# Kernel tuning notes

Measured on AMD Instinct MI355X. Metric: run time of the kernel, lower is better.

Reference implementation:

```python
import jax, jax.numpy as jnp
import numpy as np

EPS = 1e-5

def conv3(x, w, b):
    # 3x3 conv, stride 1, pad 1, NCHW/OIHW
    y = jax.lax.conv_general_dilated(x, w, (1, 1), ((1, 1), (1, 1)),
                                     dimension_numbers=('NCHW', 'OIHW', 'NCHW'))
    return y + b[None, :, None, None]

def positional_norm(x):
    # per-pixel channel-wise norm; torch .var() is unbiased (ddof=1)
    mean = jnp.mean(x, axis=1, keepdims=True)
    var = jnp.var(x, axis=1, keepdims=True, ddof=1)
    return (x - mean) / jnp.sqrt(var + EPS)

def bilinear_gather(x, py, px):
    # x: [B,C,H,W]; py/px: [B,K,H,W] absolute sample coords -> [B,C,K,H,W]
    B, C, H, W = x.shape
    K = py.shape[1]
    xf = x.reshape(B, C, H * W)
    y0 = jnp.floor(py).astype(jnp.int32)
    x0 = jnp.floor(px).astype(jnp.int32)
    wy = py - y0.astype(x.dtype)
    wx = px - x0.astype(x.dtype)

    def corner(yi, xi):
        valid = ((yi >= 0) & (yi < H) & (xi >= 0) & (xi < W)).astype(x.dtype)
        idx = (jnp.clip(yi, 0, H - 1) * W + jnp.clip(xi, 0, W - 1)).reshape(B, 1, K * H * W)
        v = jnp.take_along_axis(xf, idx, axis=2).reshape(B, C, K, H, W)
        return v * valid[:, None]

    out = ((1 - wy) * (1 - wx))[:, None] * corner(y0, x0)
    out = out + ((1 - wy) * wx)[:, None] * corner(y0, x0 + 1)
    out = out + (wy * (1 - wx))[:, None] * corner(y0 + 1, x0)
    out = out + (wy * wx)[:, None] * corner(y0 + 1, x0 + 1)
    return out

def dcn_v2(feat, cond, w_off, b_off, w_dcn, b_dcn):
    # DCNv2Pack: conv_offset(cond) -> (o1, o2, mask); modulated deformable 3x3 conv on feat
    B, C, H, W = feat.shape
    om = conv3(cond, w_off, b_off)                      # [B, 27, H, W]
    off = om[:, :18].reshape(B, 9, 2, H, W)             # (dy, dx) per kernel tap
    mask = jax.nn.sigmoid(om[:, 18:])                   # [B, 9, H, W]
    dy, dx = off[:, :, 0], off[:, :, 1]
    ki = jnp.repeat(jnp.arange(-1.0, 2.0, dtype=feat.dtype), 3)   # tap row offsets
    kj = jnp.tile(jnp.arange(-1.0, 2.0, dtype=feat.dtype), 3)     # tap col offsets
    hh = jnp.arange(H, dtype=feat.dtype)
    ww = jnp.arange(W, dtype=feat.dtype)
    py = dy + hh[None, None, :, None] + ki[None, :, None, None]
    px = dx + ww[None, None, None, :] + kj[None, :, None, None]
    sampled = bilinear_gather(feat, py, px)             # [B,C,9,H,W]
    wk = w_dcn.reshape(w_dcn.shape[0], C, 9)
    out = jnp.einsum('bkhw,bckhw,ock->bohw', mask, sampled, wk)
    return out + b_dcn[None, :, None, None]

def spade_forward(x, ref, w1, b1, w2, b2, w_off, b_off, w_dcn, b_dcn, w_g, b_g, w_be, b_be):
    normalized = positional_norm(x)
    h = jax.nn.relu(conv3(jnp.concatenate((normalized, ref), axis=1), w1, b1))
    cond = jax.nn.relu(conv3(h, w2, b2))
    ref_refine = dcn_v2(ref, cond, w_off, b_off, w_dcn, b_dcn)
    gamma = conv3(ref_refine, w_g, b_g)
    beta = conv3(ref_refine, w_be, b_be)
    return normalized * (1 + gamma) + beta

def setup_inputs() -> dict:
    key = jax.random.key(0)
    ks = jax.random.split(key, 16)
    B, NC, SC, H, W = 2, 64, 64, 96, 96
    mid = (NC + SC) // 8  # 16
    s = 0.05
    inp = {
        'x': jax.random.normal(ks[0], (B, NC, H, W), jnp.float32),
        'ref': jax.random.normal(ks[1], (B, SC, H, W), jnp.float32),
        'w1': jax.random.normal(ks[2], (mid, NC + SC, 3, 3), jnp.float32) * s,
        'b1': jax.random.normal(ks[3], (mid,), jnp.float32) * s,
        'w2': jax.random.normal(ks[4], (SC, mid, 3, 3), jnp.float32) * s,
        'b2': jax.random.normal(ks[5], (SC,), jnp.float32) * s,
        'w_off': jax.random.normal(ks[6], (27, SC, 3, 3), jnp.float32) * 0.01,
        'b_off': jax.random.normal(ks[7], (27,), jnp.float32) * 0.01,
        'w_dcn': jax.random.normal(ks[8], (SC, SC, 3, 3), jnp.float32) * s,
        'b_dcn': jax.random.normal(ks[9], (SC,), jnp.float32) * s,
        'w_g': jax.random.normal(ks[10], (NC, SC, 3, 3), jnp.float32) * s,
        'b_g': jax.random.normal(ks[11], (NC,), jnp.float32) * s,
        'w_be': jax.random.normal(ks[12], (NC, SC, 3, 3), jnp.float32) * s,
        'b_be': jax.random.normal(ks[13], (NC,), jnp.float32) * s,
    }
    return inp

def reference(x, ref, w1, b1, w2, b2, w_off, b_off, w_dcn, b_dcn, w_g, b_g, w_be, b_be):
    return spade_forward(x, ref, w1, b1, w2, b2, w_off, b_off, w_dcn, b_dcn, w_g, b_g, w_be, b_be)
```

## Files before the change

kernel.cpp:

```cpp
#include <hip/hip_runtime.h>
#include <math.h>

namespace {

typedef __attribute__((ext_vector_type(8))) short          bf16x8;
typedef __attribute__((ext_vector_type(8))) unsigned short u16x8;
typedef __attribute__((ext_vector_type(4))) float          f32x4;

constexpr int B_  = 2;
constexpr int H_  = 96;
constexpr int W_  = 96;
constexpr int HW_ = H_ * W_;
constexpr int NC_ = 64;
constexpr int SC_ = 64;

__device__ inline unsigned short f2bf(float f) {
    union { float f; unsigned u; } v; v.f = f;
    unsigned r = v.u + 0x7FFFu + ((v.u >> 16) & 1u);
    return (unsigned short)(r >> 16);
}
__device__ inline float bf2f(unsigned short s) {
    union { unsigned u; float f; } v; v.u = ((unsigned)s) << 16; return v.f;
}
__device__ inline bf16x8 ld_frag(const unsigned short* p) {
    return *reinterpret_cast<const bf16x8*>(p);
}

__global__ __launch_bounds__(256)
void prologue(const float* __restrict__ x, const float* __restrict__ ref,
              const float* __restrict__ w1, const float* __restrict__ w2,
              const float* __restrict__ woff, const float* __restrict__ wg,
              const float* __restrict__ wbe, const float* __restrict__ wdcn,
              float* __restrict__ nrm, unsigned short* __restrict__ cc,
              unsigned short* __restrict__ wt1, unsigned short* __restrict__ wt2,
              unsigned short* __restrict__ wtoff, unsigned short* __restrict__ wtg,
              unsigned short* __restrict__ wtbe, unsigned short* __restrict__ wbd) {
    __shared__ float red1[4][64];
    __shared__ float red2[4][64];
    __shared__ float rtile[64][65];

    int blk = blockIdx.x;
    int t   = threadIdx.x;

    if (blk < 288) {
        int b  = blk / 144;
        int p0 = (blk % 144) * 64;
        int px = t & 63;
        int cg = t >> 6;
        int p  = p0 + px;

        float v[16];
        float s1 = 0.f, s2 = 0.f;
        const float* xb = x + ((size_t)b * NC_ + cg * 16) * HW_ + p;
        #pragma unroll
        for (int j = 0; j < 16; ++j) {
            v[j] = xb[j * HW_];
            s1 += v[j];
            s2 = fmaf(v[j], v[j], s2);
        }
        red1[cg][px] = s1;
        red2[cg][px] = s2;

        const float* rb = ref + (size_t)b * SC_ * HW_ + p0 + px;
        #pragma unroll
        for (int it = 0; it < 16; ++it) {
            int ch = it * 4 + cg;
            rtile[ch][px] = rb[(size_t)ch * HW_];
        }
        __syncthreads();

        s1 = red1[0][px] + red1[1][px] + red1[2][px] + red1[3][px];
        s2 = red2[0][px] + red2[1][px] + red2[2][px] + red2[3][px];
        float mean = s1 * (1.f / 64.f);
        float var  = (s2 - 64.f * mean * mean) * (1.f / 63.f);
        float inv  = 1.f / sqrtf(var + 1e-5f);
        float* nb = nrm + ((size_t)b * NC_ + cg * 16) * HW_ + p;
        u16x8 pk[2];
        #pragma unroll
        for (int j = 0; j < 16; ++j) {
            float nv = (v[j] - mean) * inv;
            nb[j * HW_] = nv;
            pk[j >> 3][j & 7] = f2bf(nv);
        }
        size_t bp = (size_t)b * HW_ + p;
        *reinterpret_cast<u16x8*>(&cc[bp * 128 + cg * 16 + 0]) = pk[0];
        *reinterpret_cast<u16x8*>(&cc[bp * 128 + cg * 16 + 8]) = pk[1];

        {
            int wpx = t >> 2, q = t & 3;
            size_t bp2 = (size_t)b * HW_ + p0 + wpx;
            u16x8 o0, o1;
            #pragma unroll
            for (int j = 0; j < 8; ++j) {
                o0[j] = f2bf(rtile[q * 16 + j][wpx]);
                o1[j] = f2bf(rtile[q * 16 + 8 + j][wpx]);
            }
            *reinterpret_cast<u16x8*>(&cc[bp2 * 128 + 64 + q * 16 + 0]) = o0;
            *reinterpret_cast<u16x8*>(&cc[bp2 * 128 + 64 + q * 16 + 8]) = o1;
        }
    } else {
        int idx = (blk - 288) * 256 + t;
        if (idx < 9 * 16 * 128) {
            int tap = idx / (16 * 128), oc = (idx / 128) % 16, ic = idx % 128;
            wt1[idx] = f2bf(w1[(oc * 128 + ic) * 9 + tap]);
        }
        if (idx < 9 * 64 * 32) {
            int tap = idx / (64 * 32), oc = (idx / 32) % 64, ic = idx % 32;
            wt2[idx] = (ic < 16) ? f2bf(w2[(oc * 16 + ic) * 9 + tap]) : (unsigned short)0;
        }
        if (idx < 9 * 32 * 64) {
            int tap = idx / (32 * 64), oc = (idx / 64) % 32, ic = idx % 64;
            wtoff[idx] = (oc < 27) ? f2bf(woff[(oc * 64 + ic) * 9 + tap]) : (unsigned short)0;
        }
        if (idx < 9 * 64 * 64) {
            int tap = idx / (64 * 64), oc = (idx / 64) % 64, ic = idx % 64;
            wtg[idx]  = f2bf(wg [(oc * 64 + ic) * 9 + tap]);
            wtbe[idx] = f2bf(wbe[(oc * 64 + ic) * 9 + tap]);
        }
        if (idx < 64 * 576) {
            int oc = idx / 576, r = idx - oc * 576;
            int tap = r >> 6, ic = r & 63;
            wbd[idx] = f2bf(wdcn[oc * 576 + ic * 9 + tap]);
        }
    }
}

template <int ICS, int ICP, int COLP, int COUT_PAD, int COUT_REAL,
          bool DUAL, bool RELU, int OMODE>
__global__ __launch_bounds__(256)
void conv_bf(const unsigned short* __restrict__ in,
             const unsigned short* __restrict__ Wt,
             const unsigned short* __restrict__ Wt2,
             const float* __restrict__ bias, const float* __restrict__ bias2,
             const float* __restrict__ nrm, float* __restrict__ outF,
             unsigned short* __restrict__ outB) {
    constexpr int NOCT = COUT_PAD / 16;
    constexpr int WPO  = 4 / NOCT;
    constexpr int MTP  = NOCT;
    constexpr int NACC = DUAL ? 2 : 1;
    constexpr int NKS  = ICP / 32;
    constexpr int NCH8 = ICP / 8;

    __shared__ unsigned short patch[6 * 18 * COLP];

    int t   = threadIdx.x;
    int blk = blockIdx.x;
    int bx  = blk % 6;
    int by  = (blk / 6) % 24;
    int b   = blk / 144;
    int x0  = bx * 16, y0 = by * 4;

    for (int e = t; e < 6 * 18 * NCH8; e += 256) {
        int kc  = e % NCH8;
        int col = (e / NCH8) % 18;
        int row = e / (NCH8 * 18);
        int yy = y0 + row - 1, xx = x0 + col - 1;
        bf16x8 v = (bf16x8){0, 0, 0, 0, 0, 0, 0, 0};
        if (kc * 8 < ICS && (unsigned)yy < (unsigned)H_ && (unsigned)xx < (unsigned)W_) {
            v = ld_frag(&in[((size_t)b * HW_ + yy * W_ + xx) * ICS + kc * 8]);
        }
        *reinterpret_cast<bf16x8*>(&patch[(row * 18 + col) * COLP + kc * 8]) = v;
    }
    __syncthreads();

    int wave = t >> 6, lane = t & 63;
    int fr = lane & 15, fq = lane >> 4;
    int oct  = wave / WPO;
    int widx = wave - oct * WPO;
    int mt0  = widx * MTP;

    f32x4 acc[MTP][NACC];
    #pragma unroll
    for (int i = 0; i < MTP; ++i)
        #pragma unroll
        for (int a = 0; a < NACC; ++a)
            acc[i][a] = (f32x4){0.f, 0.f, 0.f, 0.f};

    constexpr int dyv[9] = {0,0,0,1,1,1,2,2,2};
    constexpr int dxv[9] = {0,1,2,0,1,2,0,1,2};

    #pragma unroll
    for (int tap = 0; tap < 9; ++tap) {
        int dy = dyv[tap], dx = dxv[tap];
        #pragma unroll
        for (int ks = 0; ks < NKS; ++ks) {
            const size_t wo = ((size_t)tap * COUT_PAD + oct * 16 + fr) * ICP + ks * 32 + fq * 8;
            bf16x8 wfA = ld_frag(&Wt[wo]);
            bf16x8 wfB;
            if (DUAL) wfB = ld_frag(&Wt2[wo]);
            #pragma unroll
            for (int i = 0; i < MTP; ++i) {
                bf16x8 pf = ld_frag(&patch[((mt0 + i + dy) * 18 + (fr + dx)) * COLP
                                           + ks * 32 + fq * 8]);
                acc[i][0] = __builtin_amdgcn_mfma_f32_16x16x32_bf16(wfA, pf, acc[i][0], 0, 0, 0);
                if (DUAL)
                    acc[i][1] = __builtin_amdgcn_mfma_f32_16x16x32_bf16(wfB, pf, acc[i][1], 0, 0, 0);
            }
        }
    }

    #pragma unroll
    for (int i = 0; i < MTP; ++i) {
        int py = mt0 + i;
        if (OMODE == 1) {
            size_t p = (size_t)b * HW_ + (size_t)(y0 + py) * W_ + x0 + fr;
            ushort4 sv;
            #pragma unroll
            for (int j = 0; j < 4; ++j) {
                float v = acc[i][0][j] + bias[oct * 16 + fq * 4 + j];
                if (RELU) v = fmaxf(v, 0.f);
                ((unsigned short*)&sv)[j] = f2bf(v);
            }
            *reinterpret_cast<ushort4*>(&outB[p * COUT_REAL + oct * 16 + fq * 4]) = sv;
        } else if (OMODE == 2) {
            size_t p = (size_t)b * HW_ + (size_t)(y0 + py) * W_ + x0 + fr;
            float4 o4;
            #pragma unroll
            for (int j = 0; j < 4; ++j) {
                int oc = oct * 16 + fq * 4 + j;
                float v = acc[i][0][j] + (oc < COUT_REAL ? bias[oc] : 0.f);
                ((float*)&o4)[j] = v;
            }
            *reinterpret_cast<float4*>(&outF[p * 32 + oct * 16 + fq * 4]) = o4;
        } else {
            #pragma unroll
            for (int j = 0; j < 4; ++j) {
                int oc = oct * 16 + fq * 4 + j;
                if (oc >= COUT_REAL) continue;
                size_t off = ((size_t)b * COUT_REAL + oc) * HW_
                           + (size_t)(y0 + py) * W_ + x0 + fr;
                float v = acc[i][0][j] + bias[oc];
                if (DUAL) {
                    float be = acc[i][1][j] + bias2[oc];
                    float nv = nrm[off];
                    outF[off] = fmaf(nv, 1.f + v, be);
                } else {
                    outF[off] = RELU ? fmaxf(v, 0.f) : v;
                }
            }
        }
    }
}

constexpr int SROW = 584;

__global__ __launch_bounds__(256)
void dcn_kernel(const unsigned short* __restrict__ cc, const float* __restrict__ omP,
                const unsigned short* __restrict__ wbd, const float* __restrict__ b_dcn,
                unsigned short* __restrict__ rrT) {
    __shared__ unsigned short sS[16 * SROW];
    __shared__ float4 cwL[144];
    __shared__ int4   ciL[144];

    int t  = threadIdx.x;
    int b  = blockIdx.x / 576;
    int p0 = (blockIdx.x % 576) * 16;

    const unsigned short* ccb = cc + (size_t)b * HW_ * 128;

    if (t < 144) {
        int pp = t / 9, k = t - pp * 9;
        int p  = p0 + pp;
        int y  = p / W_, x = p - y * W_;
        const float* omp = &omP[(size_t)(b * HW_ + p) * 32];
        float dy = omp[2 * k];
        float dx = omp[2 * k + 1];
        float mk = omp[18 + k];
        mk = 1.f / (1.f + expf(-mk));

        float py = dy + (float)y + (float)(k / 3 - 1);
        float px = dx + (float)x + (float)(k % 3 - 1);
        float fy = floorf(py), fx = floorf(px);
        int   y0 = (int)fy,   x0 = (int)fx;
        float wy = py - fy,   wx = px - fx;

        float cw[4];
        int   ci[4];
        #pragma unroll
        for (int i = 0; i < 4; ++i) {
            int yy = y0 + (i >> 1);
            int xx = x0 + (i & 1);
            bool valid = (yy >= 0) && (yy < H_) && (xx >= 0) && (xx < W_);
            int yc = yy < 0 ? 0 : (yy > H_ - 1 ? H_ - 1 : yy);
            int xc = xx < 0 ? 0 : (xx > W_ - 1 ? W_ - 1 : xx);
            ci[i] = yc * W_ + xc;
            float wyi = (i >> 1) ? wy : (1.f - wy);
            float wxi = (i & 1)  ? wx : (1.f - wx);
            cw[i] = valid ? mk * wyi * wxi : 0.f;
        }
        cwL[t] = make_float4(cw[0], cw[1], cw[2], cw[3]);
        ciL[t] = make_int4(ci[0], ci[1], ci[2], ci[3]);
    }
    __syncthreads();

    {
        int pp = t >> 4, cg = t & 15;
        #pragma unroll
        for (int k = 0; k < 9; ++k) {
            float4 cw = cwL[pp * 9 + k];
            int4   ci = ciL[pp * 9 + k];
            ushort4 r0 = *reinterpret_cast<const ushort4*>(&ccb[(size_t)ci.x * 128 + 64 + cg * 4]);
            ushort4 r1 = *reinterpret_cast<const ushort4*>(&ccb[(size_t)ci.y * 128 + 64 + cg * 4]);
            ushort4 r2 = *reinterpret_cast<const ushort4*>(&ccb[(size_t)ci.z * 128 + 64 + cg * 4]);
            ushort4 r3 = *reinterpret_cast<const ushort4*>(&ccb[(size_t)ci.w * 128 + 64 + cg * 4]);
            float vx = cw.x * bf2f(r0.x) + cw.y * bf2f(r1.x) + cw.z * bf2f(r2.x) + cw.w * bf2f(r3.x);
            float vy = cw.x * bf2f(r0.y) + cw.y * bf2f(r1.y) + cw.z * bf2f(r2.y) + cw.w * bf2f(r3.y);
            float vz = cw.x * bf2f(r0.z) + cw.y * bf2f(r1.z) + cw.z * bf2f(r2.z) + cw.w * bf2f(r3.z);
            float vw = cw.x * bf2f(r0.w) + cw.y * bf2f(r1.w) + cw.z * bf2f(r2.w) + cw.w * bf2f(r3.w);
            ushort4 sv;
            sv.x = f2bf(vx); sv.y = f2bf(vy); sv.z = f2bf(vz); sv.w = f2bf(vw);
            *reinterpret_cast<ushort4*>(&sS[pp * SROW + k * 64 + cg * 4]) = sv;
        }
    }
    __syncthreads();

    int wave = t >> 6, lane = t & 63;
    int fr = lane & 15, fq = lane >> 4;

    f32x4 acc = (f32x4){0.f, 0.f, 0.f, 0.f};
    for (int ks = 0; ks < 18; ++ks) {
        bf16x8 wf = ld_frag(&wbd[(size_t)(wave * 16 + fr) * 576 + ks * 32 + fq * 8]);
        bf16x8 pf = ld_frag(&sS[(size_t)fr * SROW + ks * 32 + fq * 8]);
        acc = __builtin_amdgcn_mfma_f32_16x16x32_bf16(wf, pf, acc, 0, 0, 0);
    }

    {
        size_t p = (size_t)b * HW_ + p0 + fr;
        ushort4 sv;
        #pragma unroll
        for (int j = 0; j < 4; ++j)
            ((unsigned short*)&sv)[j] = f2bf(acc[j] + b_dcn[wave * 16 + fq * 4 + j]);
        *reinterpret_cast<ushort4*>(&rrT[p * 64 + wave * 16 + fq * 4]) = sv;
    }
}

}

extern "C" void kernel_launch(void* const* d_in, const int* in_sizes, int n_in,
                              void* d_out, int out_size, void* d_ws, size_t ws_size,
                              hipStream_t stream) {
    (void)in_sizes; (void)n_in; (void)out_size; (void)ws_size;

    const float* x     = (const float*)d_in[0];
    const float* ref   = (const float*)d_in[1];
    const float* w1    = (const float*)d_in[2];
    const float* b1    = (const float*)d_in[3];
    const float* w2    = (const float*)d_in[4];
    const float* b2    = (const float*)d_in[5];
    const float* w_off = (const float*)d_in[6];
    const float* b_off = (const float*)d_in[7];
    const float* w_dcn = (const float*)d_in[8];
    const float* b_dcn = (const float*)d_in[9];
    const float* w_g   = (const float*)d_in[10];
    const float* b_g   = (const float*)d_in[11];
    const float* w_be  = (const float*)d_in[12];
    const float* b_be  = (const float*)d_in[13];

    float* out = (float*)d_out;
    float* ws  = (float*)d_ws;

    float* nrm = ws;
    float* omP = nrm + 1179648;
    unsigned short* cc    = (unsigned short*)(omP + 589824);
    unsigned short* hmidT = cc    + 2359296;
    unsigned short* condT = hmidT + 294912;
    unsigned short* rrT   = condT + 1179648;
    unsigned short* wt1   = rrT   + 1179648;
    unsigned short* wt2   = wt1   + 18432;
    unsigned short* wtoff = wt2   + 18432;
    unsigned short* wtg   = wtoff + 18432;
    unsigned short* wtbe  = wtg   + 36864;
    unsigned short* wbd   = wtbe  + 36864;

    prologue<<<432, 256, 0, stream>>>(x, ref, w1, w2, w_off, w_g, w_be, w_dcn,
                                      nrm, cc, wt1, wt2, wtoff, wtg, wtbe, wbd);

    constexpr int GRID = 288;

    conv_bf<128, 128, 136, 16, 16, false, true, 1>
        <<<GRID, 256, 0, stream>>>(cc, wt1, nullptr, b1, nullptr, nullptr, nullptr, hmidT);

    conv_bf<16, 32, 40, 64, 64, false, true, 1>
        <<<GRID, 256, 0, stream>>>(hmidT, wt2, nullptr, b2, nullptr, nullptr, nullptr, condT);

    conv_bf<64, 64, 72, 32, 27, false, false, 2>
        <<<GRID, 256, 0, stream>>>(condT, wtoff, nullptr, b_off, nullptr, nullptr, omP, nullptr);

    dcn_kernel<<<B_ * 576, 256, 0, stream>>>(cc, omP, wbd, b_dcn, rrT);

    conv_bf<64, 64, 72, 64, 64, true, false, 0>
        <<<GRID, 256, 0, stream>>>(rrT, wtg, wtbe, b_g, b_be, nrm, out, nullptr);
}
```

Measured before the change: 73.76 us.

## Double DCN pixel tile to 32, widen gathers to 16B, swizzle block order

The deformable conv kernel now processes 32 pixels per block instead of 16. Each weight fragment is reused across two MFMA accumulators, and the block count is halved. Bilinear gathers load 8 bf16 channels per thread (16-byte loads) rather than 4, and block indices are swizzled across groups of 8 to spread neighbouring tiles. The LDS footprint roughly doubles, which may lower occupancy, and the grid shrinks to 576 blocks.

Result: faster. 68.44 us (-7.2%).

```diff
diff --git a/kernel.cpp b/kernel.cpp
--- a/kernel.cpp
+++ b/kernel.cpp
@@ -243,23 +243,26 @@
 }
 
 constexpr int SROW = 584;
+constexpr int DT   = 32;
 
 __global__ __launch_bounds__(256)
 void dcn_kernel(const unsigned short* __restrict__ cc, const float* __restrict__ omP,
                 const unsigned short* __restrict__ wbd, const float* __restrict__ b_dcn,
                 unsigned short* __restrict__ rrT) {
-    __shared__ unsigned short sS[16 * SROW];
-    __shared__ float4 cwL[144];
-    __shared__ int4   ciL[144];
-
-    int t  = threadIdx.x;
-    int b  = blockIdx.x / 576;
-    int p0 = (blockIdx.x % 576) * 16;
+    __shared__ unsigned short sS[DT * SROW];
+    __shared__ float4 cwL[DT * 9];
+    __shared__ int4   ciL[DT * 9];
+
+    int t = threadIdx.x;
+    int bid = blockIdx.x;
+    int swz = (bid & 7) * 72 + (bid >> 3);
+    int b   = swz / (HW_ / DT);
+    int p0  = (swz % (HW_ / DT)) * DT;
 
     const unsigned short* ccb = cc + (size_t)b * HW_ * 128;
 
-    if (t < 144) {
-        int pp = t / 9, k = t - pp * 9;
+    for (int e = t; e < DT * 9; e += 256) {
+        int pp = e / 9, k = e - pp * 9;
         int p  = p0 + pp;
         int y  = p / W_, x = p - y * W_;
         const float* omp = &omP[(size_t)(b * HW_ + p) * 32];
@@ -288,28 +291,29 @@
             float wxi = (i & 1)  ? wx : (1.f - wx);
             cw[i] = valid ? mk * wyi * wxi : 0.f;
         }
-        cwL[t] = make_float4(cw[0], cw[1], cw[2], cw[3]);
-        ciL[t] = make_int4(ci[0], ci[1], ci[2], ci[3]);
+        cwL[e] = make_float4(cw[0], cw[1], cw[2], cw[3]);
+        ciL[e] = make_int4(ci[0], ci[1], ci[2], ci[3]);
     }
     __syncthreads();
 
     {
-        int pp = t >> 4, cg = t & 15;
+        int pp = t >> 3, cg8 = t & 7;
         #pragma unroll
         for (int k = 0; k < 9; ++k) {
             float4 cw = cwL[pp * 9 + k];
             int4   ci = ciL[pp * 9 + k];
-            ushort4 r0 = *reinterpret_cast<const ushort4*>(&ccb[(size_t)ci.x * 128 + 64 + cg * 4]);
-            ushort4 r1 = *reinterpret_cast<const ushort4*>(&ccb[(size_t)ci.y * 128 + 64 + cg * 4]);
-            ushort4 r2 = *reinterpret_cast<const ushort4*>(&ccb[(size_t)ci.z * 128 + 64 + cg * 4]);
-            ushort4 r3 = *reinterpret_cast<const ushort4*>(&ccb[(size_t)ci.w * 128 + 64 + cg * 4]);
-            float vx = cw.x * bf2f(r0.x) + cw.y * bf2f(r1.x) + cw.z * bf2f(r2.x) + cw.w * bf2f(r3.x);
-            float vy = cw.x * bf2f(r0.y) + cw.y * bf2f(r1.y) + cw.z * bf2f(r2.y) + cw.w * bf2f(r3.y);
-            float vz = cw.x * bf2f(r0.z) + cw.y * bf2f(r1.z) + cw.z * bf2f(r2.z) + cw.w * bf2f(r3.z);
-            float vw = cw.x * bf2f(r0.w) + cw.y * bf2f(r1.w) + cw.z * bf2f(r2.w) + cw.w * bf2f(r3.w);
-            ushort4 sv;
-            sv.x = f2bf(vx); sv.y = f2bf(vy); sv.z = f2bf(vz); sv.w = f2bf(vw);
-            *reinterpret_cast<ushort4*>(&sS[pp * SROW + k * 64 + cg * 4]) = sv;
+            u16x8 r0 = *reinterpret_cast<const u16x8*>(&ccb[(size_t)ci.x * 128 + 64 + cg8 * 8]);
+            u16x8 r1 = *reinterpret_cast<const u16x8*>(&ccb[(size_t)ci.y * 128 + 64 + cg8 * 8]);
+            u16x8 r2 = *reinterpret_cast<const u16x8*>(&ccb[(size_t)ci.z * 128 + 64 + cg8 * 8]);
+            u16x8 r3 = *reinterpret_cast<const u16x8*>(&ccb[(size_t)ci.w * 128 + 64 + cg8 * 8]);
+            u16x8 sv;
+            #pragma unroll
+            for (int j = 0; j < 8; ++j) {
+                float v = cw.x * bf2f(r0[j]) + cw.y * bf2f(r1[j])
+                        + cw.z * bf2f(r2[j]) + cw.w * bf2f(r3[j]);
+                sv[j] = f2bf(v);
+            }
+            *reinterpret_cast<u16x8*>(&sS[pp * SROW + k * 64 + cg8 * 8]) = sv;
         }
     }
     __syncthreads();
@@ -317,20 +321,27 @@
     int wave = t >> 6, lane = t & 63;
     int fr = lane & 15, fq = lane >> 4;
 
-    f32x4 acc = (f32x4){0.f, 0.f, 0.f, 0.f};
+    f32x4 acc0 = (f32x4){0.f, 0.f, 0.f, 0.f};
+    f32x4 acc1 = (f32x4){0.f, 0.f, 0.f, 0.f};
     for (int ks = 0; ks < 18; ++ks) {
-        bf16x8 wf = ld_frag(&wbd[(size_t)(wave * 16 + fr) * 576 + ks * 32 + fq * 8]);
-        bf16x8 pf = ld_frag(&sS[(size_t)fr * SROW + ks * 32 + fq * 8]);
-        acc = __builtin_amdgcn_mfma_f32_16x16x32_bf16(wf, pf, acc, 0, 0, 0);
+        bf16x8 wf  = ld_frag(&wbd[(size_t)(wave * 16 + fr) * 576 + ks * 32 + fq * 8]);
+        bf16x8 pf0 = ld_frag(&sS[(size_t)fr * SROW + ks * 32 + fq * 8]);
+        bf16x8 pf1 = ld_frag(&sS[(size_t)(16 + fr) * SROW + ks * 32 + fq * 8]);
+        acc0 = __builtin_amdgcn_mfma_f32_16x16x32_bf16(wf, pf0, acc0, 0, 0, 0);
+        acc1 = __builtin_amdgcn_mfma_f32_16x16x32_bf16(wf, pf1, acc1, 0, 0, 0);
     }
 
     {
         size_t p = (size_t)b * HW_ + p0 + fr;
-        ushort4 sv;
-        #pragma unroll
-        for (int j = 0; j < 4; ++j)
-            ((unsigned short*)&sv)[j] = f2bf(acc[j] + b_dcn[wave * 16 + fq * 4 + j]);
-        *reinterpret_cast<ushort4*>(&rrT[p * 64 + wave * 16 + fq * 4]) = sv;
+        ushort4 sv0, sv1;
+        #pragma unroll
+        for (int j = 0; j < 4; ++j) {
+            float bo = b_dcn[wave * 16 + fq * 4 + j];
+            ((unsigned short*)&sv0)[j] = f2bf(acc0[j] + bo);
+            ((unsigned short*)&sv1)[j] = f2bf(acc1[j] + bo);
+        }
+        *reinterpret_cast<ushort4*>(&rrT[p * 64 + wave * 16 + fq * 4]) = sv0;
+        *reinterpret_cast<ushort4*>(&rrT[(p + 16) * 64 + wave * 16 + fq * 4]) = sv1;
     }
 }
 
@@ -386,7 +397,7 @@
     conv_bf<64, 64, 72, 32, 27, false, false, 2>
         <<<GRID, 256, 0, stream>>>(condT, wtoff, nullptr, b_off, nullptr, nullptr, omP, nullptr);
 
-    dcn_kernel<<<B_ * 576, 256, 0, stream>>>(cc, omP, wbd, b_dcn, rrT);
+    dcn_kernel<<<B_ * (HW_ / DT), 256, 0, stream>>>(cc, omP, wbd, b_dcn, rrT);
 
     conv_bf<64, 64, 72, 64, 64, true, false, 0>
         <<<GRID, 256, 0, stream>>>(rrT, wtg, wtbe, b_g, b_be, nrm, out, nullptr);
```
